# Kernel tuning notes

Measured on AMD Instinct MI355X. Metric: run time of the kernel, lower is better.

The kernel has to match this reference:

```python
import jax, jax.numpy as jnp
import numpy as np

B = 2097152  # number of Gaussians


def setup_inputs() -> dict:
    key = jax.random.key(0)
    k1, k2, k3, k4, k5, k6 = jax.random.split(key, 6)
    return {
        "loc1": jax.random.normal(k1, (B, 3), dtype=jnp.float32),
        "scale1": jax.random.uniform(k2, (B, 3), dtype=jnp.float32),
        "rot_matrix1": jax.random.normal(k3, (B, 3, 3), dtype=jnp.float32),
        "loc2": jax.random.normal(k4, (B, 3), dtype=jnp.float32),
        "scale2": jax.random.uniform(k5, (B, 3), dtype=jnp.float32),
        "rot_matrix2": jax.random.normal(k6, (B, 3, 3), dtype=jnp.float32),
    }


def reference(loc1, scale1, rot_matrix1, loc2, scale2, rot_matrix2):
    # ||mu1 - mu2||^2  -> (B,)
    loc_diff2 = jnp.sum((loc1 - loc2) ** 2, axis=-1)

    # cov2 = R2 diag(scale2) R2^T  -> (B,3,3)
    cov2 = jnp.einsum("bij,bj,bkj->bik", rot_matrix2, scale2, rot_matrix2)
    # cov2 rotated into frame of Gaussian 1: R1^T cov2 R1  -> (B,3,3)
    cov2_R1 = jnp.einsum("bji,bjk,bkl->bil", rot_matrix1, cov2, rot_matrix1)

    # E = diag(sqrt(s1)) cov2_R1 diag(sqrt(s1)), then symmetrize
    s1_sqrt = jnp.sqrt(scale1)  # (B,3)
    E = s1_sqrt[:, :, None] * cov2_R1 * s1_sqrt[:, None, :]
    E = (E + jnp.swapaxes(E, 1, 2)) * 0.5

    # trace of matrix sqrt via eigenvalues: sum (lambda^2)^(1/4) = sum |lambda|^(1/2)
    E_eig = jnp.linalg.eigvalsh(E)  # (B,3)
    E_sqrt_trace = jnp.sum(jnp.sqrt(jnp.sqrt(E_eig ** 2)), axis=-1)

    cov_wasserstein = jnp.sum(scale1, axis=-1) + jnp.sum(scale2, axis=-1) - 2.0 * E_sqrt_trace
    cov_wasserstein = jnp.maximum(cov_wasserstein, 0.0)
    return jnp.sqrt(loc_diff2 + cov_wasserstein)
```

## Files before the change

kernel.cpp:

```cpp
#include <hip/hip_runtime.h>
#include <math.h>

#define BLK  256
#define GRID 1024

struct Elem {
    float l1x, l1y, l1z, l2x, l2y, l2z;
    float s1a, s1b, s1c, s2a, s2b, s2c;
    float R1[9], R2[9];
};

__device__ __forceinline__ void load_elem(
    Elem& e, long long i,
    const float* __restrict__ loc1, const float* __restrict__ scale1,
    const float* __restrict__ rot1, const float* __restrict__ loc2,
    const float* __restrict__ scale2, const float* __restrict__ rot2)
{
    const float* p;
    p = loc1 + i * 3;   e.l1x = p[0]; e.l1y = p[1]; e.l1z = p[2];
    p = loc2 + i * 3;   e.l2x = p[0]; e.l2y = p[1]; e.l2z = p[2];
    p = scale1 + i * 3; e.s1a = p[0]; e.s1b = p[1]; e.s1c = p[2];
    p = scale2 + i * 3; e.s2a = p[0]; e.s2b = p[1]; e.s2c = p[2];
    p = rot1 + i * 9;
#pragma unroll
    for (int k = 0; k < 9; ++k) e.R1[k] = p[k];
    p = rot2 + i * 9;
#pragma unroll
    for (int k = 0; k < 9; ++k) e.R2[k] = p[k];
}

__device__ __forceinline__ float compute_elem(const Elem& e)
{
    const float dx = e.l1x - e.l2x, dy = e.l1y - e.l2y, dz = e.l1z - e.l2z;
    const float loc_diff2 = dx * dx + dy * dy + dz * dz;

    const float s1a = e.s1a, s1b = e.s1b, s1c = e.s1c;
    const float s2a = e.s2a, s2b = e.s2b, s2c = e.s2c;
    const float* R1 = e.R1;
    const float* R2 = e.R2;

    const float m00 = s2a * R2[0] * R2[0] + s2b * R2[1] * R2[1] + s2c * R2[2] * R2[2];
    const float m01 = s2a * R2[0] * R2[3] + s2b * R2[1] * R2[4] + s2c * R2[2] * R2[5];
    const float m02 = s2a * R2[0] * R2[6] + s2b * R2[1] * R2[7] + s2c * R2[2] * R2[8];
    const float m11 = s2a * R2[3] * R2[3] + s2b * R2[4] * R2[4] + s2c * R2[5] * R2[5];
    const float m12 = s2a * R2[3] * R2[6] + s2b * R2[4] * R2[7] + s2c * R2[5] * R2[8];
    const float m22 = s2a * R2[6] * R2[6] + s2b * R2[7] * R2[7] + s2c * R2[8] * R2[8];

    float A[9];
    A[0] = m00 * R1[0] + m01 * R1[3] + m02 * R1[6];
    A[1] = m00 * R1[1] + m01 * R1[4] + m02 * R1[7];
    A[2] = m00 * R1[2] + m01 * R1[5] + m02 * R1[8];
    A[3] = m01 * R1[0] + m11 * R1[3] + m12 * R1[6];
    A[4] = m01 * R1[1] + m11 * R1[4] + m12 * R1[7];
    A[5] = m01 * R1[2] + m11 * R1[5] + m12 * R1[8];
    A[6] = m02 * R1[0] + m12 * R1[3] + m22 * R1[6];
    A[7] = m02 * R1[1] + m12 * R1[4] + m22 * R1[7];
    A[8] = m02 * R1[2] + m12 * R1[5] + m22 * R1[8];

    float T[9];
    T[0] = R1[0] * A[0] + R1[3] * A[3] + R1[6] * A[6];
    T[1] = R1[0] * A[1] + R1[3] * A[4] + R1[6] * A[7];
    T[2] = R1[0] * A[2] + R1[3] * A[5] + R1[6] * A[8];
    T[3] = R1[1] * A[0] + R1[4] * A[3] + R1[7] * A[6];
    T[4] = R1[1] * A[1] + R1[4] * A[4] + R1[7] * A[7];
    T[5] = R1[1] * A[2] + R1[4] * A[5] + R1[7] * A[8];
    T[6] = R1[2] * A[0] + R1[5] * A[3] + R1[8] * A[6];
    T[7] = R1[2] * A[1] + R1[5] * A[4] + R1[8] * A[7];
    T[8] = R1[2] * A[2] + R1[5] * A[5] + R1[8] * A[8];

    const float sq0 = __builtin_amdgcn_sqrtf(s1a);
    const float sq1 = __builtin_amdgcn_sqrtf(s1b);
    const float sq2 = __builtin_amdgcn_sqrtf(s1c);
    const float e00 = s1a * T[0];
    const float e11 = s1b * T[4];
    const float e22 = s1c * T[8];
    const float e01 = 0.5f * sq0 * sq1 * (T[1] + T[3]);
    const float e02 = 0.5f * sq0 * sq2 * (T[2] + T[6]);
    const float e12 = 0.5f * sq1 * sq2 * (T[5] + T[7]);

    const float q  = (e00 + e11 + e22) * (1.0f / 3.0f);
    const float p1 = e01 * e01 + e02 * e02 + e12 * e12;
    const float d0 = e00 - q, d1 = e11 - q, d2 = e22 - q;
    const float p2 = d0 * d0 + d1 * d1 + d2 * d2 + 2.0f * p1;

    float trace_sqrt;
    if (p2 > 1e-24f) {
        const float p   = __builtin_amdgcn_sqrtf(p2 * (1.0f / 6.0f));
        const float inv = __builtin_amdgcn_rcpf(p);
        const float b00 = d0 * inv, b11 = d1 * inv, b22 = d2 * inv;
        const float b01 = e01 * inv, b02 = e02 * inv, b12 = e12 * inv;
        float detB = b00 * (b11 * b22 - b12 * b12)
                   - b01 * (b01 * b22 - b12 * b02)
                   + b02 * (b01 * b12 - b11 * b02);
        float r = 0.5f * detB;
        r = fminf(fmaxf(r, -1.0f), 1.0f);

        const float ax = fabsf(r);
        const float z  = __builtin_amdgcn_sqrtf(1.0f - ax);
        const float w  = z * (1.5707288f + ax * (-0.2121144f
                           + ax * (0.0742610f + ax * (-0.0187293f))));
        const float ac = (r >= 0.0f) ? w : (3.14159265358979f - w);

        const float phi = ac * (1.0f / 3.0f);
        const float c   = __cosf(phi);
        const float s   = __sinf(phi);
        const float twop = 2.0f * p;
        const float eig1 = q + twop * c;
        const float eig3 = q + twop * (-0.5f * c - 0.86602540378f * s);
        const float eig2 = 3.0f * q - eig1 - eig3;
        trace_sqrt = __builtin_amdgcn_sqrtf(fabsf(eig1))
                   + __builtin_amdgcn_sqrtf(fabsf(eig2))
                   + __builtin_amdgcn_sqrtf(fabsf(eig3));
    } else {
        trace_sqrt = 3.0f * __builtin_amdgcn_sqrtf(fabsf(q));
    }

    float cov_w = (s1a + s1b + s1c) + (s2a + s2b + s2c) - 2.0f * trace_sqrt;
    cov_w = fmaxf(cov_w, 0.0f);
    return __builtin_amdgcn_sqrtf(loc_diff2 + cov_w);
}

__global__ __launch_bounds__(BLK, 4) void wasserstein_kernel(
    const float* __restrict__ loc1,   const float* __restrict__ scale1,
    const float* __restrict__ rot1,   const float* __restrict__ loc2,
    const float* __restrict__ scale2, const float* __restrict__ rot2,
    float* __restrict__ out, int B)
{
    const long long stride = (long long)GRID * BLK;
    long long idx = (long long)blockIdx.x * BLK + threadIdx.x;
    const int nPer = B / (GRID * BLK);

    if ((nPer & 1) == 0 && nPer >= 2) {
        Elem a, b;
        load_elem(a, idx, loc1, scale1, rot1, loc2, scale2, rot2);
        const int pairs = nPer >> 1;
        for (int p = 0; p < pairs - 1; ++p) {
            load_elem(b, idx + stride, loc1, scale1, rot1, loc2, scale2, rot2);
            out[idx] = compute_elem(a);
            load_elem(a, idx + 2 * stride, loc1, scale1, rot1, loc2, scale2, rot2);
            out[idx + stride] = compute_elem(b);
            idx += 2 * stride;
        }
        load_elem(b, idx + stride, loc1, scale1, rot1, loc2, scale2, rot2);
        out[idx] = compute_elem(a);
        out[idx + stride] = compute_elem(b);
    } else {
        for (long long i = idx; i < B; i += stride) {
            Elem a;
            load_elem(a, i, loc1, scale1, rot1, loc2, scale2, rot2);
            out[i] = compute_elem(a);
        }
    }
}

extern "C" void kernel_launch(void* const* d_in, const int* in_sizes, int n_in,
                              void* d_out, int out_size, void* d_ws, size_t ws_size,
                              hipStream_t stream) {
    const float* loc1   = (const float*)d_in[0];
    const float* scale1 = (const float*)d_in[1];
    const float* rot1   = (const float*)d_in[2];
    const float* loc2   = (const float*)d_in[3];
    const float* scale2 = (const float*)d_in[4];
    const float* rot2   = (const float*)d_in[5];
    float* out = (float*)d_out;

    const int B = in_sizes[0] / 3;

    wasserstein_kernel<<<GRID, BLK, 0, stream>>>(loc1, scale1, rot1,
                                                 loc2, scale2, rot2, out, B);
}
```

Before: 242.2 us.

## Vectorize loads with four elements per thread and nontemporal 128-bit accesses

Replaces the grid-stride loop with a one-shot grid where each thread processes four consecutive elements. All inputs are fetched as aligned float4 nontemporal loads and the output is written with a single float4 nontemporal store. The launch-bounds hint is relaxed to allow more registers per thread. Tail handling for sizes not divisible by the block×elements product is removed, so correctness depends on B being a multiple of 1024.

```diff
diff --git a/kernel.cpp b/kernel.cpp
--- a/kernel.cpp
+++ b/kernel.cpp
@@ -1,43 +1,22 @@
 #include <hip/hip_runtime.h>
 #include <math.h>
 
-#define BLK  256
-#define GRID 1024
+#define BLK 256
+#define EPT 4
 
-struct Elem {
-    float l1x, l1y, l1z, l2x, l2y, l2z;
-    float s1a, s1b, s1c, s2a, s2b, s2c;
-    float R1[9], R2[9];
-};
+typedef float v4f __attribute__((ext_vector_type(4)));
 
-__device__ __forceinline__ void load_elem(
-    Elem& e, long long i,
-    const float* __restrict__ loc1, const float* __restrict__ scale1,
-    const float* __restrict__ rot1, const float* __restrict__ loc2,
-    const float* __restrict__ scale2, const float* __restrict__ rot2)
-{
-    const float* p;
-    p = loc1 + i * 3;   e.l1x = p[0]; e.l1y = p[1]; e.l1z = p[2];
-    p = loc2 + i * 3;   e.l2x = p[0]; e.l2y = p[1]; e.l2z = p[2];
-    p = scale1 + i * 3; e.s1a = p[0]; e.s1b = p[1]; e.s1c = p[2];
-    p = scale2 + i * 3; e.s2a = p[0]; e.s2b = p[1]; e.s2c = p[2];
-    p = rot1 + i * 9;
-#pragma unroll
-    for (int k = 0; k < 9; ++k) e.R1[k] = p[k];
-    p = rot2 + i * 9;
-#pragma unroll
-    for (int k = 0; k < 9; ++k) e.R2[k] = p[k];
+__device__ __forceinline__ v4f nt4(const float* p) {
+    return __builtin_nontemporal_load(reinterpret_cast<const v4f*>(p));
 }
 
-__device__ __forceinline__ float compute_elem(const Elem& e)
+__device__ __forceinline__ float compute_elem(
+    float l1x, float l1y, float l1z, float l2x, float l2y, float l2z,
+    float s1a, float s1b, float s1c, float s2a, float s2b, float s2c,
+    const float* __restrict__ R1, const float* __restrict__ R2)
 {
-    const float dx = e.l1x - e.l2x, dy = e.l1y - e.l2y, dz = e.l1z - e.l2z;
+    const float dx = l1x - l2x, dy = l1y - l2y, dz = l1z - l2z;
     const float loc_diff2 = dx * dx + dy * dy + dz * dz;
-
-    const float s1a = e.s1a, s1b = e.s1b, s1c = e.s1c;
-    const float s2a = e.s2a, s2b = e.s2b, s2c = e.s2c;
-    const float* R1 = e.R1;
-    const float* R2 = e.R2;
 
     const float m00 = s2a * R2[0] * R2[0] + s2b * R2[1] * R2[1] + s2c * R2[2] * R2[2];
     const float m01 = s2a * R2[0] * R2[3] + s2b * R2[1] * R2[4] + s2c * R2[2] * R2[5];
@@ -120,37 +99,75 @@
     return __builtin_amdgcn_sqrtf(loc_diff2 + cov_w);
 }
 
-__global__ __launch_bounds__(BLK, 4) void wasserstein_kernel(
+__global__ __launch_bounds__(BLK, 2) void wasserstein_kernel(
     const float* __restrict__ loc1,   const float* __restrict__ scale1,
     const float* __restrict__ rot1,   const float* __restrict__ loc2,
     const float* __restrict__ scale2, const float* __restrict__ rot2,
-    float* __restrict__ out, int B)
+    float* __restrict__ out)
 {
-    const long long stride = (long long)GRID * BLK;
-    long long idx = (long long)blockIdx.x * BLK + threadIdx.x;
-    const int nPer = B / (GRID * BLK);
+    const long long t  = (long long)blockIdx.x * BLK + threadIdx.x;
+    const long long e0 = t * EPT;
 
-    if ((nPer & 1) == 0 && nPer >= 2) {
-        Elem a, b;
-        load_elem(a, idx, loc1, scale1, rot1, loc2, scale2, rot2);
-        const int pairs = nPer >> 1;
-        for (int p = 0; p < pairs - 1; ++p) {
-            load_elem(b, idx + stride, loc1, scale1, rot1, loc2, scale2, rot2);
-            out[idx] = compute_elem(a);
-            load_elem(a, idx + 2 * stride, loc1, scale1, rot1, loc2, scale2, rot2);
-            out[idx + stride] = compute_elem(b);
-            idx += 2 * stride;
+    const float* gL1 = loc1   + e0 * 3;
+    const float* gL2 = loc2   + e0 * 3;
+    const float* gS1 = scale1 + e0 * 3;
+    const float* gS2 = scale2 + e0 * 3;
+    const float* gR1 = rot1   + e0 * 9;
+    const float* gR2 = rot2   + e0 * 9;
+
+    const v4f r2a = nt4(gR2 +  0), r2b = nt4(gR2 +  4), r2c = nt4(gR2 +  8);
+    const v4f r2d = nt4(gR2 + 12), r2e = nt4(gR2 + 16), r2f = nt4(gR2 + 20);
+    const v4f r2g = nt4(gR2 + 24), r2h = nt4(gR2 + 28), r2i = nt4(gR2 + 32);
+    const v4f r1a = nt4(gR1 +  0), r1b = nt4(gR1 +  4), r1c = nt4(gR1 +  8);
+    const v4f r1d = nt4(gR1 + 12), r1e = nt4(gR1 + 16), r1f = nt4(gR1 + 20);
+    const v4f r1g = nt4(gR1 + 24), r1h = nt4(gR1 + 28), r1i = nt4(gR1 + 32);
+    const v4f s2x = nt4(gS2 + 0), s2y = nt4(gS2 + 4), s2z = nt4(gS2 + 8);
+    const v4f s1x = nt4(gS1 + 0), s1y = nt4(gS1 + 4), s1z = nt4(gS1 + 8);
+    const v4f l1a = nt4(gL1 + 0), l1b = nt4(gL1 + 4), l1c = nt4(gL1 + 8);
+    const v4f l2a = nt4(gL2 + 0), l2b = nt4(gL2 + 4), l2c = nt4(gL2 + 8);
+
+    float L1[12], L2[12], S1[12], S2[12], Q1[36], Q2[36];
+    {
+        const v4f a[3] = {l1a, l1b, l1c};
+        const v4f b[3] = {l2a, l2b, l2c};
+        const v4f c[3] = {s1x, s1y, s1z};
+        const v4f d[3] = {s2x, s2y, s2z};
+#pragma unroll
+        for (int j = 0; j < 3; ++j) {
+#pragma unroll
+            for (int q = 0; q < 4; ++q) {
+                L1[4*j+q] = a[j][q];
+                L2[4*j+q] = b[j][q];
+                S1[4*j+q] = c[j][q];
+                S2[4*j+q] = d[j][q];
+            }
         }
-        load_elem(b, idx + stride, loc1, scale1, rot1, loc2, scale2, rot2);
-        out[idx] = compute_elem(a);
-        out[idx + stride] = compute_elem(b);
-    } else {
-        for (long long i = idx; i < B; i += stride) {
-            Elem a;
-            load_elem(a, i, loc1, scale1, rot1, loc2, scale2, rot2);
-            out[i] = compute_elem(a);
+        const v4f e[9] = {r1a, r1b, r1c, r1d, r1e, r1f, r1g, r1h, r1i};
+        const v4f f[9] = {r2a, r2b, r2c, r2d, r2e, r2f, r2g, r2h, r2i};
+#pragma unroll
+        for (int j = 0; j < 9; ++j) {
+#pragma unroll
+            for (int q = 0; q < 4; ++q) {
+                Q1[4*j+q] = e[j][q];
+                Q2[4*j+q] = f[j][q];
+            }
         }
     }
+
+    float of[EPT];
+#pragma unroll
+    for (int k = 0; k < EPT; ++k) {
+        of[k] = compute_elem(
+            L1[3*k], L1[3*k+1], L1[3*k+2],
+            L2[3*k], L2[3*k+1], L2[3*k+2],
+            S1[3*k], S1[3*k+1], S1[3*k+2],
+            S2[3*k], S2[3*k+1], S2[3*k+2],
+            Q1 + 9*k, Q2 + 9*k);
+    }
+
+    v4f o;
+    o[0] = of[0]; o[1] = of[1]; o[2] = of[2]; o[3] = of[3];
+    __builtin_nontemporal_store(o, reinterpret_cast<v4f*>(out + e0));
 }
 
 extern "C" void kernel_launch(void* const* d_in, const int* in_sizes, int n_in,
@@ -165,7 +182,8 @@
     float* out = (float*)d_out;
 
     const int B = in_sizes[0] / 3;
+    const int grid = B / (BLK * EPT);
 
-    wasserstein_kernel<<<GRID, BLK, 0, stream>>>(loc1, scale1, rot1,
-                                                 loc2, scale2, rot2, out, B);
+    wasserstein_kernel<<<grid, BLK, 0, stream>>>(loc1, scale1, rot1,
+                                                 loc2, scale2, rot2, out);
 }
```

New measurement: 286.5 us. +18.3%, slower.

## Drop manual double-buffering and raise occupancy with larger grid

Applied to the files above, without the earlier changes.

Removes the two-element software pipelining in the grid-stride loop and uses a simple one-element-per-iteration loop. The grid doubles and launch bounds request 8 waves per SIMD instead of 4, so memory latency is hidden by more resident threads rather than by explicit prefetch registers. This risks exposing load latency per thread and may add register spilling under the tighter bound.

```diff
diff --git a/kernel.cpp b/kernel.cpp
--- a/kernel.cpp
+++ b/kernel.cpp
@@ -2,42 +2,27 @@
 #include <math.h>
 
 #define BLK  256
-#define GRID 1024
+#define GRID 2048
 
-struct Elem {
-    float l1x, l1y, l1z, l2x, l2y, l2z;
-    float s1a, s1b, s1c, s2a, s2b, s2c;
-    float R1[9], R2[9];
-};
+struct F3 { float x, y, z; };
 
-__device__ __forceinline__ void load_elem(
-    Elem& e, long long i,
-    const float* __restrict__ loc1, const float* __restrict__ scale1,
-    const float* __restrict__ rot1, const float* __restrict__ loc2,
-    const float* __restrict__ scale2, const float* __restrict__ rot2)
-{
-    const float* p;
-    p = loc1 + i * 3;   e.l1x = p[0]; e.l1y = p[1]; e.l1z = p[2];
-    p = loc2 + i * 3;   e.l2x = p[0]; e.l2y = p[1]; e.l2z = p[2];
-    p = scale1 + i * 3; e.s1a = p[0]; e.s1b = p[1]; e.s1c = p[2];
-    p = scale2 + i * 3; e.s2a = p[0]; e.s2b = p[1]; e.s2c = p[2];
-    p = rot1 + i * 9;
-#pragma unroll
-    for (int k = 0; k < 9; ++k) e.R1[k] = p[k];
-    p = rot2 + i * 9;
-#pragma unroll
-    for (int k = 0; k < 9; ++k) e.R2[k] = p[k];
+__device__ __forceinline__ F3 ldF3(const float* p) {
+    F3 r; r.x = p[0]; r.y = p[1]; r.z = p[2]; return r;
 }
 
-__device__ __forceinline__ float compute_elem(const Elem& e)
+__device__ __forceinline__ float compute_elem(
+    const F3 L1, const F3 L2, const F3 S1, const F3 S2,
+    const F3 r1a, const F3 r1b, const F3 r1c,
+    const F3 r2a, const F3 r2b, const F3 r2c)
 {
-    const float dx = e.l1x - e.l2x, dy = e.l1y - e.l2y, dz = e.l1z - e.l2z;
+    const float dx = L1.x - L2.x, dy = L1.y - L2.y, dz = L1.z - L2.z;
     const float loc_diff2 = dx * dx + dy * dy + dz * dz;
 
-    const float s1a = e.s1a, s1b = e.s1b, s1c = e.s1c;
-    const float s2a = e.s2a, s2b = e.s2b, s2c = e.s2c;
-    const float* R1 = e.R1;
-    const float* R2 = e.R2;
+    const float s1a = S1.x, s1b = S1.y, s1c = S1.z;
+    const float s2a = S2.x, s2b = S2.y, s2c = S2.z;
+
+    const float R1[9] = {r1a.x, r1a.y, r1a.z, r1b.x, r1b.y, r1b.z, r1c.x, r1c.y, r1c.z};
+    const float R2[9] = {r2a.x, r2a.y, r2a.z, r2b.x, r2b.y, r2b.z, r2c.x, r2c.y, r2c.z};
 
     const float m00 = s2a * R2[0] * R2[0] + s2b * R2[1] * R2[1] + s2c * R2[2] * R2[2];
     const float m01 = s2a * R2[0] * R2[3] + s2b * R2[1] * R2[4] + s2c * R2[2] * R2[5];
@@ -120,36 +105,28 @@
     return __builtin_amdgcn_sqrtf(loc_diff2 + cov_w);
 }
 
-__global__ __launch_bounds__(BLK, 4) void wasserstein_kernel(
+__global__ __launch_bounds__(BLK, 8) void wasserstein_kernel(
     const float* __restrict__ loc1,   const float* __restrict__ scale1,
     const float* __restrict__ rot1,   const float* __restrict__ loc2,
     const float* __restrict__ scale2, const float* __restrict__ rot2,
     float* __restrict__ out, int B)
 {
     const long long stride = (long long)GRID * BLK;
-    long long idx = (long long)blockIdx.x * BLK + threadIdx.x;
-    const int nPer = B / (GRID * BLK);
+    const long long start  = (long long)blockIdx.x * BLK + threadIdx.x;
 
-    if ((nPer & 1) == 0 && nPer >= 2) {
-        Elem a, b;
-        load_elem(a, idx, loc1, scale1, rot1, loc2, scale2, rot2);
-        const int pairs = nPer >> 1;
-        for (int p = 0; p < pairs - 1; ++p) {
-            load_elem(b, idx + stride, loc1, scale1, rot1, loc2, scale2, rot2);
-            out[idx] = compute_elem(a);
-            load_elem(a, idx + 2 * stride, loc1, scale1, rot1, loc2, scale2, rot2);
-            out[idx + stride] = compute_elem(b);
-            idx += 2 * stride;
-        }
-        load_elem(b, idx + stride, loc1, scale1, rot1, loc2, scale2, rot2);
-        out[idx] = compute_elem(a);
-        out[idx + stride] = compute_elem(b);
-    } else {
-        for (long long i = idx; i < B; i += stride) {
-            Elem a;
-            load_elem(a, i, loc1, scale1, rot1, loc2, scale2, rot2);
-            out[i] = compute_elem(a);
-        }
+    for (long long i = start; i < B; i += stride) {
+        const F3 L1  = ldF3(loc1   + i * 3);
+        const F3 L2  = ldF3(loc2   + i * 3);
+        const F3 S1  = ldF3(scale1 + i * 3);
+        const F3 S2  = ldF3(scale2 + i * 3);
+        const F3 r1a = ldF3(rot1 + i * 9);
+        const F3 r1b = ldF3(rot1 + i * 9 + 3);
+        const F3 r1c = ldF3(rot1 + i * 9 + 6);
+        const F3 r2a = ldF3(rot2 + i * 9);
+        const F3 r2b = ldF3(rot2 + i * 9 + 3);
+        const F3 r2c = ldF3(rot2 + i * 9 + 6);
+
+        out[i] = compute_elem(L1, L2, S1, S2, r1a, r1b, r1c, r2a, r2b, r2c);
     }
 }
 
```

After: 242.6 us. No clear change (+0.2%).
